# Optimization experiments

Hardware: AMD Instinct MI355X
Metric: run time of the kernel (lower is better)

Reference implementation:

```python
import jax, jax.numpy as jnp
import numpy as np
from jax import lax

B, T, N, HID = 4, 144, 256, 64
CH, NC = 9, 4  # chunk_size_short, num_chunks_short


def setup_inputs():
    key = jax.random.key(0)
    ks = jax.random.split(key, 30)
    r = lambda i, sh, s=0.05: jax.random.normal(ks[i], sh, jnp.float32) * s
    adj = (jax.random.uniform(ks[1], (N, N)) < 0.1).astype(jnp.float32)
    adj = adj.at[jnp.arange(N), jnp.arange(N)].set(1.0)  # self-loops
    return {
        "seg": jax.random.normal(ks[0], (B, T, N, N), jnp.float32),
        "adj": adj,
        "dist": jax.random.uniform(ks[2], (N, N), jnp.float32),
        "W_gat": r(3, (N, HID)),
        "a_src": r(4, (HID,)),
        "a_dst": r(5, (HID,)),
        "lstm_Wih": r(6, (4 * HID, HID)),
        "lstm_Whh": r(7, (4 * HID, HID)),
        "lstm_bih": r(8, (4 * HID,)),
        "lstm_bhh": r(9, (4 * HID,)),
        "attnL_W": r(10, (HID, HID)),
        "attnL_b": r(11, (HID,)),
        "attnL_v": r(12, (HID,)),
        "gru_Wih": r(13, (NC, 3 * HID, HID)),
        "gru_Whh": r(14, (NC, 3 * HID, HID)),
        "gru_bih": r(15, (NC, 3 * HID)),
        "gru_bhh": r(16, (NC, 3 * HID)),
        "attnS_W": r(17, (NC, HID, HID)),
        "attnS_b": r(18, (NC, HID)),
        "attnS_v": r(19, (NC, HID)),
        "lin1_W": r(20, (2 * HID, HID + HID * NC)),
        "lin1_b": r(21, (2 * HID,)),
        "lin2_W": r(22, (N * N, 2 * HID)),
        "lin2_b": r(23, (N * N,)),
        "conv_k": r(24, (1, 1, 3, 3)),
        "conv_b": r(25, (1,)),
    }


def gat_features(seg, adj, dist, W_gat, a_src, a_dst):
    # Batches the per-timestep GAT over the time axis (B,T folded together).
    Wh = jnp.einsum('btnf,fh->btnh', seg, W_gat)                     # (B,T,N,H)
    e = jax.nn.leaky_relu((Wh @ a_src)[..., :, None] + (Wh @ a_dst)[..., None, :], 0.2)
    e = e - dist                                                     # distance penalty on logits
    logits = jnp.where(adj > 0, e, -1e9)                             # mask non-edges
    attn = jax.nn.softmax(logits, axis=-1)                           # (B,T,N,N)
    Hn = jax.nn.elu(jnp.einsum('btij,btjh->btih', attn, Wh))         # (B,T,N,H)
    return Hn.mean(axis=2)                                           # (B,T,H) mean-pool over nodes


def lstm(x, Wih, Whh, bih, bhh):
    h0 = jnp.zeros((x.shape[0], Whh.shape[1]), x.dtype)
    def step(carry, xt):
        h, c = carry
        g = xt @ Wih.T + bih + h @ Whh.T + bhh
        i, f, gg, o = jnp.split(g, 4, axis=-1)  # torch gate order i,f,g,o
        c = jax.nn.sigmoid(f) * c + jax.nn.sigmoid(i) * jnp.tanh(gg)
        h = jax.nn.sigmoid(o) * jnp.tanh(c)
        return (h, c), h
    _, ys = lax.scan(step, (h0, h0), jnp.swapaxes(x, 0, 1))
    return jnp.swapaxes(ys, 0, 1)


def gru(x, Wih, Whh, bih, bhh):
    h0 = jnp.zeros((x.shape[0], Whh.shape[1]), x.dtype)
    def step(h, xt):
        gx = xt @ Wih.T + bih
        gh = h @ Whh.T + bhh
        xr, xz, xn = jnp.split(gx, 3, axis=-1)  # torch gate order r,z,n
        hr, hz, hn = jnp.split(gh, 3, axis=-1)
        rr = jax.nn.sigmoid(xr + hr)
        zz = jax.nn.sigmoid(xz + hz)
        nn_ = jnp.tanh(xn + rr * hn)
        h = (1.0 - zz) * nn_ + zz * h
        return h, h
    _, ys = lax.scan(step, h0, jnp.swapaxes(x, 0, 1))
    return jnp.swapaxes(ys, 0, 1)


def tattn(h, W, b, v):
    s = jnp.tanh(h @ W + b) @ v          # (B,T) additive attention scores
    a = jax.nn.softmax(s, axis=1)
    return jnp.einsum('bt,bth->bh', a, h)


def reference(seg, adj, dist, W_gat, a_src, a_dst, lstm_Wih, lstm_Whh, lstm_bih, lstm_bhh,
              attnL_W, attnL_b, attnL_v, gru_Wih, gru_Whh, gru_bih, gru_bhh,
              attnS_W, attnS_b, attnS_v, lin1_W, lin1_b, lin2_W, lin2_b, conv_k, conv_b):
    Bsz = seg.shape[0]
    feats = gat_features(seg, adj, dist, W_gat, a_src, a_dst)        # (B,T,H)
    ctxL = tattn(lstm(feats, lstm_Wih, lstm_Whh, lstm_bih, lstm_bhh), attnL_W, attnL_b, attnL_v)
    # Short-term GCN features are the same GAT outputs on the last W_short steps.
    short = feats[:, -CH * NC:, :].reshape(Bsz, NC, CH, HID)
    gru_out = jax.vmap(gru, in_axes=(1, 0, 0, 0, 0), out_axes=1)(short, gru_Wih, gru_Whh, gru_bih, gru_bhh)
    ctxS = jax.vmap(tattn, in_axes=(1, 0, 0, 0), out_axes=1)(gru_out, attnS_W, attnS_b, attnS_v)  # (B,NC,H)
    fused = jnp.concatenate([ctxL, ctxS.reshape(Bsz, NC * HID)], axis=1)  # (B, 5H)
    h1 = jax.nn.relu(fused @ lin1_W.T + lin1_b)
    out = (h1 @ lin2_W.T + lin2_b).reshape(Bsz, 1, N, N)
    out = lax.conv_general_dilated(out, conv_k, (1, 1), 'SAME',
                                   dimension_numbers=('NCHW', 'OIHW', 'NCHW'))
    out = out + conv_b[None, :, None, None]
    return jax.nn.softplus(out[:, 0])
```

## Files before the change

kernel.cpp:

```cpp
#include <hip/hip_runtime.h>
#include <hip/hip_bf16.h>
#include <cstddef>


typedef __attribute__((ext_vector_type(8))) short bf16x8;
typedef __attribute__((ext_vector_type(4))) float f32x4;

__device__ __forceinline__ float sigf(float x) { return 1.0f / (1.0f + __expf(-x)); }
__device__ __forceinline__ float tanh_(float x) {
    x = fminf(fmaxf(x, -15.f), 15.f);
    float e = __expf(2.f * x);
    return (e - 1.f) / (e + 1.f);
}
__device__ __forceinline__ unsigned short f2b(float f) {
    unsigned u = __float_as_uint(f);
    u += 0x7FFFu + ((u >> 16) & 1u);
    return (unsigned short)(u >> 16);
}
__device__ __forceinline__ unsigned pk2(float lo, float hi) {
    __hip_bfloat162 h = __float22bfloat162_rn(float2{lo, hi});
    return *reinterpret_cast<unsigned*>(&h);
}
__device__ __forceinline__ float b2f(short s) {
    return __uint_as_float(((unsigned)(unsigned short)s) << 16);
}
__device__ __forceinline__ float rlane(float v, int k) {
    return __uint_as_float(__builtin_amdgcn_readlane(__float_as_uint(v), k));
}

__global__ void k_prep(const float* __restrict__ adj, const float* __restrict__ dist,
                       const float* __restrict__ W_gat,
                       unsigned short* __restrict__ Mb, unsigned short* __restrict__ Wt) {
    int blk = blockIdx.x, tid = threadIdx.x;
    if (blk < 256) {
        int i = blk * 256 + tid;
        Mb[i] = f2b((adj[i] > 0.f) ? -dist[i] : -1e9f);
    } else {
        for (int it = 0; it < 64; ++it) {
            int e = it * 256 + tid;
            int k = e >> 6, c = e & 63;
            Wt[c * 256 + k] = f2b(W_gat[e]);
        }
    }
}

__global__ __launch_bounds__(256, 6) void k_gatA(
    const float* __restrict__ seg, const unsigned short* __restrict__ Wt,
    const float* __restrict__ a_src, const float* __restrict__ a_dst,
    unsigned short* __restrict__ WhT, float* __restrict__ svec, float* __restrict__ dvec,
    float* __restrict__ smaxp, float* __restrict__ dmaxp) {
    __shared__ __align__(16) short A_s[64 * 64];
    __shared__ float red[8];

    const int tid  = threadIdx.x;
    const int lane = tid & 63;
    const int wv   = tid >> 6;
    const int blk  = blockIdx.x;
    const int bt   = blk >> 2;
    const int sub  = blk & 3;
    const float* __restrict__ segp = seg + (size_t)bt * 65536 + sub * 64 * 256;

    f32x4 acc[4];
    #pragma unroll
    for (int n = 0; n < 4; ++n) acc[n] = (f32x4)(0.f);

    for (int kc = 0; kc < 4; ++kc) {
        #pragma unroll
        for (int it = 0; it < 2; ++it) {
            int unit = it * 256 + tid;
            int row = unit >> 3, u = unit & 7;
            const float* g = segp + row * 256 + kc * 64 + u * 8;
            f32x4 v0 = *(const f32x4*)g;
            f32x4 v1 = *(const f32x4*)(g + 4);
            uint4 pk;
            pk.x = pk2(v0[0], v0[1]); pk.y = pk2(v0[2], v0[3]);
            pk.z = pk2(v1[0], v1[1]); pk.w = pk2(v1[2], v1[3]);
            *(uint4*)&A_s[(row * 8 + (u ^ (row & 7))) * 8] = pk;
        }
        bf16x8 bfr[2][4];
        #pragma unroll
        for (int kt2 = 0; kt2 < 2; ++kt2) {
            int ku = kt2 * 4 + (lane >> 4);
            #pragma unroll
            for (int nt = 0; nt < 4; ++nt) {
                int col = nt * 16 + (lane & 15);
                bfr[kt2][nt] = *(const bf16x8*)(Wt + col * 256 + kc * 64 + ku * 8);
            }
        }
        __syncthreads();
        int arow = wv * 16 + (lane & 15);
        #pragma unroll
        for (int kt2 = 0; kt2 < 2; ++kt2) {
            int ku = kt2 * 4 + (lane >> 4);
            bf16x8 afr = *(const bf16x8*)&A_s[(arow * 8 + (ku ^ (arow & 7))) * 8];
            #pragma unroll
            for (int nt = 0; nt < 4; ++nt)
                acc[nt] = __builtin_amdgcn_mfma_f32_16x16x32_bf16(afr, bfr[kt2][nt], acc[nt], 0, 0, 0);
        }
        __syncthreads();
    }

    float asv[4], adv[4];
    #pragma unroll
    for (int nt = 0; nt < 4; ++nt) {
        asv[nt] = a_src[nt * 16 + (lane & 15)];
        adv[nt] = a_dst[nt * 16 + (lane & 15)];
    }
    float mxs = -3e38f, mxd = -3e38f;
    int rowbase = sub * 64 + wv * 16;
    #pragma unroll
    for (int r = 0; r < 4; ++r) {
        float ps = acc[0][r] * asv[0] + acc[1][r] * asv[1] + acc[2][r] * asv[2] + acc[3][r] * asv[3];
        float pd = acc[0][r] * adv[0] + acc[1][r] * adv[1] + acc[2][r] * adv[2] + acc[3][r] * adv[3];
        #pragma unroll
        for (int m = 1; m < 16; m <<= 1) { ps += __shfl_xor(ps, m); pd += __shfl_xor(pd, m); }
        if ((lane & 15) == 0) {
            int row = rowbase + (lane >> 4) * 4 + r;
            svec[bt * 256 + row] = ps;
            dvec[bt * 256 + row] = pd;
        }
        mxs = fmaxf(mxs, ps); mxd = fmaxf(mxd, pd);
    }
    mxs = fmaxf(mxs, __shfl_xor(mxs, 16)); mxs = fmaxf(mxs, __shfl_xor(mxs, 32));
    mxd = fmaxf(mxd, __shfl_xor(mxd, 16)); mxd = fmaxf(mxd, __shfl_xor(mxd, 32));
    if (lane == 0) { red[wv] = mxs; red[4 + wv] = mxd; }

    {
        int c = lane & 15, q = lane >> 4;
        int kt2  = wv >> 1;
        int oct  = (wv & 1) * 2 + (q >> 1);
        int laneP = oct * 16 + c;
        int e0b  = (q & 1) * 8;
        #pragma unroll
        for (int nt = 0; nt < 4; ++nt) {
            uint2 pk4;
            pk4.x = pk2(acc[nt][0], acc[nt][1]);
            pk4.y = pk2(acc[nt][2], acc[nt][3]);
            *(uint2*)((char*)A_s + (((kt2 * 4 + nt) * 64 + laneP) * 16 + e0b)) = pk4;
        }
    }
    __syncthreads();
    {
        const uint4* Fs = (const uint4*)A_s;
        uint4* Gd = (uint4*)(WhT + (size_t)bt * 16384 + sub * 4096);
        Gd[tid] = Fs[tid];
        Gd[256 + tid] = Fs[256 + tid];
    }
    if (tid == 0) {
        smaxp[blk] = fmaxf(fmaxf(red[0], red[1]), fmaxf(red[2], red[3]));
        dmaxp[blk] = fmaxf(fmaxf(red[4], red[5]), fmaxf(red[6], red[7]));
    }
}

__global__ __launch_bounds__(256, 4) void k_gatB(
    const unsigned short* __restrict__ WhT, const float* __restrict__ svec,
    const float* __restrict__ dvec, const float* __restrict__ smaxp,
    const float* __restrict__ dmaxp, const unsigned short* __restrict__ Mb,
    float* __restrict__ fpart) {
    __shared__ __align__(16) float dv_l[256];
    __shared__ float red[256];

    const int tid  = threadIdx.x;
    const int lane = tid & 63;
    const int wv   = tid >> 6;
    const int blk  = blockIdx.x;
    const int bt   = blk >> 2;
    const int sub  = blk & 3;
    const unsigned short* __restrict__ Wp = WhT + (size_t)bt * 16384;

    dv_l[tid] = dvec[bt * 256 + tid];
    float mB;
    {
        float ms = fmaxf(fmaxf(smaxp[bt * 4], smaxp[bt * 4 + 1]),
                         fmaxf(smaxp[bt * 4 + 2], smaxp[bt * 4 + 3]));
        float md = fmaxf(fmaxf(dmaxp[bt * 4], dmaxp[bt * 4 + 1]),
                         fmaxf(dmaxp[bt * 4 + 2], dmaxp[bt * 4 + 3]));
        float x = ms + md;
        mB = fmaxf(x, 0.2f * x);
    }
    const int prow = sub * 64 + wv * 16 + (lane & 15);
    const float sv = svec[bt * 256 + prow];
    __syncthreads();

    f32x4 acc2[4];
    #pragma unroll
    for (int n = 0; n < 4; ++n) acc2[n] = (f32x4)(0.f);
    float psum = 0.f;
    const int jbase = (lane >> 4) * 8;

    #pragma unroll 1
    for (int kt = 0; kt < 8; ++kt) {
        int j0 = kt * 32 + jbase;
        bf16x8 bfr[4];
        #pragma unroll
        for (int nt = 0; nt < 4; ++nt)
            bfr[nt] = *(const bf16x8*)(Wp + ((kt * 4 + nt) * 64 + lane) * 8);
        bf16x8 mrow = *(const bf16x8*)(Mb + prow * 256 + j0);
        f32x4 d0 = *(const f32x4*)&dv_l[j0];
        f32x4 d1 = *(const f32x4*)&dv_l[j0 + 4];
        float p[8];
        #pragma unroll
        for (int e = 0; e < 4; ++e) {
            float u = sv + d0[e];
            u = fmaxf(u, 0.2f * u);
            p[e] = __expf(u + b2f(mrow[e]) - mB);
            float w = sv + d1[e];
            w = fmaxf(w, 0.2f * w);
            p[4 + e] = __expf(w + b2f(mrow[4 + e]) - mB);
        }
        psum += ((p[0] + p[1]) + (p[2] + p[3])) + ((p[4] + p[5]) + (p[6] + p[7]));
        uint4 upf;
        upf.x = pk2(p[0], p[1]); upf.y = pk2(p[2], p[3]);
        upf.z = pk2(p[4], p[5]); upf.w = pk2(p[6], p[7]);
        bf16x8 pf = *reinterpret_cast<bf16x8*>(&upf);
        #pragma unroll
        for (int nt = 0; nt < 4; ++nt)
            acc2[nt] = __builtin_amdgcn_mfma_f32_16x16x32_bf16(pf, bfr[nt], acc2[nt], 0, 0, 0);
    }
    psum += __shfl_xor(psum, 16);
    psum += __shfl_xor(psum, 32);

    float part[4] = {0.f, 0.f, 0.f, 0.f};
    #pragma unroll
    for (int r = 0; r < 4; ++r) {
        float rs  = __shfl(psum, ((lane >> 4) << 2) + r);
        float inv = 1.0f / rs;
        #pragma unroll
        for (int nt = 0; nt < 4; ++nt) {
            float x = acc2[nt][r] * inv;
            x = (x > 0.f) ? x : expm1f(x);
            part[nt] += x;
        }
    }
    #pragma unroll
    for (int nt = 0; nt < 4; ++nt) {
        part[nt] += __shfl_xor(part[nt], 16);
        part[nt] += __shfl_xor(part[nt], 32);
    }
    if ((lane >> 4) == 0) {
        #pragma unroll
        for (int nt = 0; nt < 4; ++nt) red[wv * 64 + nt * 16 + lane] = part[nt];
    }
    __syncthreads();
    if (tid < 64)
        fpart[blk * 64 + tid] = red[tid] + red[64 + tid] + red[128 + tid] + red[192 + tid];
}

__global__ __launch_bounds__(256) void k_feats(
    const float* __restrict__ fpart, const float* __restrict__ lWih,
    const float* __restrict__ lbih, const float* __restrict__ lbhh,
    float* __restrict__ feats, float* __restrict__ gx) {
    __shared__ __align__(16) float fl[64];
    int bt = blockIdx.x, tid = threadIdx.x;
    if (tid < 64) {
        float f = (fpart[(bt * 4 + 0) * 64 + tid] + fpart[(bt * 4 + 1) * 64 + tid]
                 + fpart[(bt * 4 + 2) * 64 + tid] + fpart[(bt * 4 + 3) * 64 + tid]) * (1.0f / 256.0f);
        feats[bt * 64 + tid] = f;
        fl[tid] = f;
    }
    __syncthreads();
    float a = lbih[tid] + lbhh[tid];
    const float* wp = lWih + tid * 64;
    #pragma unroll
    for (int k4 = 0; k4 < 16; ++k4) {
        f32x4 w = *(const f32x4*)(wp + k4 * 4);
        f32x4 x = *(const f32x4*)&fl[k4 * 4];
        a += w[0] * x[0] + w[1] * x[1] + w[2] * x[2] + w[3] * x[3];
    }
    gx[bt * 256 + tid] = a;
}

__global__ __launch_bounds__(256) void k_rnn(
    const float* __restrict__ gx, const float* __restrict__ lWhh, float* __restrict__ lout,
    const float* __restrict__ feats, const float* __restrict__ gWih,
    const float* __restrict__ gWhh, const float* __restrict__ gbih,
    const float* __restrict__ gbhh, float* __restrict__ gout) {
    int tid = threadIdx.x;
    if (blockIdx.x < 4) {
        int b = blockIdx.x;
        int lane = tid & 63;
        __shared__ __align__(16) float gl[2][256];
        float wr[64];
        #pragma unroll
        for (int q = 0; q < 16; ++q)
            *(f32x4*)&wr[q * 4] = *(const f32x4*)&lWhh[tid * 64 + q * 4];
        float c_s = 0.f;
        float hprev = 0.f;
        float gx_cur = gx[(size_t)b * 36864 + tid];
        for (int t = 0; t < 144; ++t) {
            float gx_next = (t < 143) ? gx[((size_t)b * 144 + t + 1) * 256 + tid] : 0.f;
            float s0 = 0.f, s1 = 0.f, s2 = 0.f, s3 = 0.f;
            #pragma unroll
            for (int k = 0; k < 64; k += 4) {
                s0 += wr[k]     * rlane(hprev, k);
                s1 += wr[k + 1] * rlane(hprev, k + 1);
                s2 += wr[k + 2] * rlane(hprev, k + 2);
                s3 += wr[k + 3] * rlane(hprev, k + 3);
            }
            float a = gx_cur + ((s0 + s1) + (s2 + s3));
            gl[t & 1][tid] = a;
            __syncthreads();
            float ig = gl[t & 1][lane],       fg = gl[t & 1][64 + lane],
                  gg = gl[t & 1][128 + lane], og = gl[t & 1][192 + lane];
            c_s = sigf(fg) * c_s + sigf(ig) * tanh_(gg);
            float h = sigf(og) * tanh_(c_s);
            hprev = h;
            if (tid < 64) lout[(b * 144 + t) * 64 + lane] = h;
            gx_cur = gx_next;
        }
    } else {
        int bi_ = blockIdx.x - 4;
        int b = bi_ >> 2, c2 = bi_ & 3;
        __shared__ float hvg[64], xvg[64], gxl[192], ghl[192];
        float wi[64], wh[64], bi = 0.f, bh = 0.f, h_s = 0.f;
        if (tid < 192) {
            #pragma unroll
            for (int q = 0; q < 16; ++q) {
                *(f32x4*)&wi[q * 4] = *(const f32x4*)&gWih[(size_t)(c2 * 192 + tid) * 64 + q * 4];
                *(f32x4*)&wh[q * 4] = *(const f32x4*)&gWhh[(size_t)(c2 * 192 + tid) * 64 + q * 4];
            }
            bi = gbih[c2 * 192 + tid];
            bh = gbhh[c2 * 192 + tid];
        }
        if (tid < 64) hvg[tid] = 0.f;
        __syncthreads();
        for (int s = 0; s < 9; ++s) {
            int t = 108 + c2 * 9 + s;
            if (tid < 64) xvg[tid] = feats[(b * 144 + t) * 64 + tid];
            __syncthreads();
            if (tid < 192) {
                float ax = bi, ah = bh;
                float a0 = 0.f, a1 = 0.f, b0 = 0.f, b1 = 0.f;
                #pragma unroll
                for (int k = 0; k < 64; k += 2) {
                    a0 += wi[k] * xvg[k];     a1 += wi[k + 1] * xvg[k + 1];
                    b0 += wh[k] * hvg[k];     b1 += wh[k + 1] * hvg[k + 1];
                }
                gxl[tid] = ax + a0 + a1; ghl[tid] = ah + b0 + b1;
            }
            __syncthreads();
            if (tid < 64) {
                float xr = gxl[tid], xz = gxl[64 + tid], xn = gxl[128 + tid];
                float hr = ghl[tid], hz = ghl[64 + tid], hn = ghl[128 + tid];
                float rr = sigf(xr + hr), zz = sigf(xz + hz);
                float nn = tanh_(xn + rr * hn);
                h_s = (1.f - zz) * nn + zz * h_s;
                hvg[tid] = h_s;
                gout[((b * 4 + c2) * 9 + s) * 64 + tid] = h_s;
            }
            __syncthreads();
        }
    }
}

__global__ __launch_bounds__(256) void k_ctx(
    const float* __restrict__ lout, const float* __restrict__ aLW,
    const float* __restrict__ aLb, const float* __restrict__ aLv,
    const float* __restrict__ gout, const float* __restrict__ aSW,
    const float* __restrict__ aSb, const float* __restrict__ aSv,
    float* __restrict__ ctxL, float* __restrict__ ctxS) {
    int tid = threadIdx.x;
    if (blockIdx.x < 4) {
        int b = blockIdx.x;
        int wv = tid >> 6, lane = tid & 63;
        __shared__ __align__(16) float Hl[144 * 64];
        __shared__ float sc[144];
        __shared__ float al[144];
        for (int i = tid; i < 9216; i += 256) Hl[i] = lout[b * 9216 + i];
        float wcol[64];
        #pragma unroll
        for (int k = 0; k < 64; ++k) wcol[k] = aLW[k * 64 + lane];
        float bb = aLb[lane], vv = aLv[lane];
        __syncthreads();
        for (int g = 0; g < 36; ++g) {
            int t = g * 4 + wv;
            float acc = bb;
            #pragma unroll
            for (int q = 0; q < 16; ++q) {
                f32x4 h4 = *(const f32x4*)&Hl[t * 64 + q * 4];
                acc += wcol[q * 4 + 0] * h4[0] + wcol[q * 4 + 1] * h4[1]
                     + wcol[q * 4 + 2] * h4[2] + wcol[q * 4 + 3] * h4[3];
            }
            float p = tanh_(acc) * vv;
            #pragma unroll
            for (int m = 1; m < 64; m <<= 1) p += __shfl_xor(p, m);
            if (lane == 0) sc[t] = p;
        }
        __syncthreads();
        float mx = -3e38f;
        for (int t2 = 0; t2 < 144; ++t2) mx = fmaxf(mx, sc[t2]);
        float ss = 0.f;
        for (int t2 = 0; t2 < 144; ++t2) ss += __expf(sc[t2] - mx);
        float inv = 1.f / ss;
        if (tid < 144) al[tid] = __expf(sc[tid] - mx) * inv;
        __syncthreads();
        if (tid < 64) {
            float acc = 0.f;
            for (int t2 = 0; t2 < 144; ++t2) acc += al[t2] * Hl[t2 * 64 + tid];
            ctxL[b * 64 + tid] = acc;
        }
    } else {
        int bi_ = blockIdx.x - 4;
        int b = bi_ >> 2, c2 = bi_ & 3;
        __shared__ float xv2[64];
        if (tid < 64) {
            int lane = tid;
            const float* Wc = aSW + c2 * 4096;
            float wcol[64];
            #pragma unroll
            for (int k = 0; k < 64; ++k) wcol[k] = Wc[k * 64 + lane];
            float bb = aSb[c2 * 64 + lane], vv = aSv[c2 * 64 + lane];
            float sv[9], hl[9];
            #pragma unroll 1
            for (int s = 0; s < 9; ++s) {
                float h = gout[((size_t)((b * 4 + c2) * 9 + s)) * 64 + lane];
                hl[s] = h;
                xv2[lane] = h;
                float acc = bb;
                #pragma unroll
                for (int k = 0; k < 64; ++k) acc += wcol[k] * xv2[k];
                float p = tanh_(acc) * vv;
                #pragma unroll
                for (int m = 1; m < 64; m <<= 1) p += __shfl_xor(p, m);
                sv[s] = p;
            }
            float mx = -3e38f;
            #pragma unroll
            for (int s = 0; s < 9; ++s) mx = fmaxf(mx, sv[s]);
            float ss = 0.f;
            #pragma unroll
            for (int s = 0; s < 9; ++s) { sv[s] = __expf(sv[s] - mx); ss += sv[s]; }
            float inv = 1.f / ss;
            float acc = 0.f;
            #pragma unroll
            for (int s = 0; s < 9; ++s) acc += sv[s] * inv * hl[s];
            ctxS[(b * 4 + c2) * 64 + lane] = acc;
        }
    }
}

__global__ __launch_bounds__(512) void k_lin1(
    const float* __restrict__ ctxL, const float* __restrict__ ctxS,
    const float* __restrict__ W, const float* __restrict__ bb,
    float* __restrict__ h1) {
    int tid = threadIdx.x;
    __shared__ __align__(16) float fu[4 * 320];
    for (int c = tid; c < 1280; c += 512) {
        int b2 = c / 320, k = c % 320;
        fu[c] = (k < 64) ? ctxL[b2 * 64 + k] : ctxS[b2 * 256 + (k - 64)];
    }
    __syncthreads();
    int b = tid >> 7, r = tid & 127;
    float acc = bb[r];
    #pragma unroll 4
    for (int k4 = 0; k4 < 80; ++k4) {
        f32x4 w = *(const f32x4*)&W[r * 320 + k4 * 4];
        f32x4 x = *(const f32x4*)&fu[b * 320 + k4 * 4];
        acc += w[0] * x[0] + w[1] * x[1] + w[2] * x[2] + w[3] * x[3];
    }
    h1[b * 128 + r] = fmaxf(acc, 0.f);
}

__global__ __launch_bounds__(256) void k_lin2(
    const float* __restrict__ h1, const float* __restrict__ W,
    const float* __restrict__ bb, float* __restrict__ h2) {
    __shared__ __align__(16) float h1l[512];
    int tid = threadIdx.x, blk = blockIdx.x;
    for (int c = tid; c < 512; c += 256) h1l[c] = h1[c];
    __syncthreads();
    int r = blk * 64 + (tid >> 2);
    int q = tid & 3;
    const float* wp = W + (size_t)r * 128 + q * 32;
    float a0 = 0.f, a1 = 0.f, a2 = 0.f, a3 = 0.f;
    #pragma unroll
    for (int i = 0; i < 8; ++i) {
        f32x4 w  = *(const f32x4*)(wp + i * 4);
        f32x4 x0 = *(const f32x4*)&h1l[q * 32 + i * 4];
        f32x4 x1 = *(const f32x4*)&h1l[128 + q * 32 + i * 4];
        f32x4 x2 = *(const f32x4*)&h1l[256 + q * 32 + i * 4];
        f32x4 x3 = *(const f32x4*)&h1l[384 + q * 32 + i * 4];
        a0 += w[0] * x0[0] + w[1] * x0[1] + w[2] * x0[2] + w[3] * x0[3];
        a1 += w[0] * x1[0] + w[1] * x1[1] + w[2] * x1[2] + w[3] * x1[3];
        a2 += w[0] * x2[0] + w[1] * x2[1] + w[2] * x2[2] + w[3] * x2[3];
        a3 += w[0] * x3[0] + w[1] * x3[1] + w[2] * x3[2] + w[3] * x3[3];
    }
    a0 += __shfl_xor(a0, 1); a0 += __shfl_xor(a0, 2);
    a1 += __shfl_xor(a1, 1); a1 += __shfl_xor(a1, 2);
    a2 += __shfl_xor(a2, 1); a2 += __shfl_xor(a2, 2);
    a3 += __shfl_xor(a3, 1); a3 += __shfl_xor(a3, 2);
    if (q == 0) {
        float bv = bb[r];
        h2[r]             = a0 + bv;
        h2[65536 + r]     = a1 + bv;
        h2[2 * 65536 + r] = a2 + bv;
        h2[3 * 65536 + r] = a3 + bv;
    }
}

__global__ __launch_bounds__(256) void k_conv(
    const float* __restrict__ h2, const float* __restrict__ ck,
    const float* __restrict__ cb, float* __restrict__ out) {
    int x = threadIdx.x;
    int b = blockIdx.x >> 8, y = blockIdx.x & 255;
    float kk[9];
    #pragma unroll
    for (int i = 0; i < 9; ++i) kk[i] = ck[i];
    const float* base = h2 + b * 65536;
    float acc = cb[0];
    #pragma unroll
    for (int dy = -1; dy <= 1; ++dy) {
        int yy = y + dy;
        if (yy < 0 || yy > 255) continue;
        #pragma unroll
        for (int dx = -1; dx <= 1; ++dx) {
            int xx = x + dx;
            if (xx < 0 || xx > 255) continue;
            acc += base[yy * 256 + xx] * kk[(dy + 1) * 3 + (dx + 1)];
        }
    }
    float r = (acc > 20.f) ? acc : log1pf(__expf(acc));
    out[b * 65536 + y * 256 + x] = r;
}

extern "C" void kernel_launch(void* const* d_in, const int* in_sizes, int n_in,
                              void* d_out, int out_size, void* d_ws, size_t ws_size,
                              hipStream_t stream) {
    const float* seg   = (const float*)d_in[0];
    const float* adj   = (const float*)d_in[1];
    const float* dist  = (const float*)d_in[2];
    const float* W_gat = (const float*)d_in[3];
    const float* a_src = (const float*)d_in[4];
    const float* a_dst = (const float*)d_in[5];
    const float* lWih  = (const float*)d_in[6];
    const float* lWhh  = (const float*)d_in[7];
    const float* lbih  = (const float*)d_in[8];
    const float* lbhh  = (const float*)d_in[9];
    const float* aLW   = (const float*)d_in[10];
    const float* aLb   = (const float*)d_in[11];
    const float* aLv   = (const float*)d_in[12];
    const float* gWih  = (const float*)d_in[13];
    const float* gWhh  = (const float*)d_in[14];
    const float* gbih  = (const float*)d_in[15];
    const float* gbhh  = (const float*)d_in[16];
    const float* aSW   = (const float*)d_in[17];
    const float* aSb   = (const float*)d_in[18];
    const float* aSv   = (const float*)d_in[19];
    const float* l1W   = (const float*)d_in[20];
    const float* l1b   = (const float*)d_in[21];
    const float* l2W   = (const float*)d_in[22];
    const float* l2b   = (const float*)d_in[23];
    const float* ck    = (const float*)d_in[24];
    const float* cb    = (const float*)d_in[25];
    float* out = (float*)d_out;

    float* ws = (float*)d_ws;
    unsigned short* Mb  = (unsigned short*)ws;
    unsigned short* Wt  = (unsigned short*)(ws + 32768);
    float* svec  = ws + 40960;
    float* dvec  = svec + 147456;
    float* smaxp = dvec + 147456;
    float* dmaxp = smaxp + 2304;
    unsigned short* WhT = (unsigned short*)(dmaxp + 2304);
    float* fpart = dmaxp + 2304 + 4718592;
    float* feats = fpart + 147456;
    float* gx    = feats + 36864;
    float* lout  = gx + 147456;
    float* gout  = lout + 36864;
    float* ctxL  = gout + 9216;
    float* ctxS  = ctxL + 256;
    float* h1    = ctxS + 1024;
    float* h2    = h1 + 512;

    k_prep<<<257, 256, 0, stream>>>(adj, dist, W_gat, Mb, Wt);
    k_gatA<<<2304, 256, 0, stream>>>(seg, Wt, a_src, a_dst, WhT, svec, dvec, smaxp, dmaxp);
    k_gatB<<<2304, 256, 0, stream>>>(WhT, svec, dvec, smaxp, dmaxp, Mb, fpart);
    k_feats<<<576, 256, 0, stream>>>(fpart, lWih, lbih, lbhh, feats, gx);
    k_rnn<<<20, 256, 0, stream>>>(gx, lWhh, lout, feats, gWih, gWhh, gbih, gbhh, gout);
    k_ctx<<<20, 256, 0, stream>>>(lout, aLW, aLb, aLv, gout, aSW, aSb, aSv, ctxL, ctxS);
    k_lin1<<<1, 512, 0, stream>>>(ctxL, ctxS, l1W, l1b, h1);
    k_lin2<<<1024, 256, 0, stream>>>(h1, l2W, l2b, h2);
    k_conv<<<1024, 256, 0, stream>>>(h2, ck, cb, out);
}
```

Measured before the change: 231.4 us.

## Fuse GAT aggregation with LSTM input projection, and RNN with attention context

```diff
diff --git a/kernel.cpp b/kernel.cpp
--- a/kernel.cpp
+++ b/kernel.cpp
@@ -152,20 +152,21 @@
     }
 }
 
-__global__ __launch_bounds__(256, 4) void k_gatB(
+__global__ __launch_bounds__(256, 4) void k_gatBF(
     const unsigned short* __restrict__ WhT, const float* __restrict__ svec,
     const float* __restrict__ dvec, const float* __restrict__ smaxp,
     const float* __restrict__ dmaxp, const unsigned short* __restrict__ Mb,
-    float* __restrict__ fpart) {
+    const float* __restrict__ lWih, const float* __restrict__ lbih,
+    const float* __restrict__ lbhh, float* __restrict__ feats, float* __restrict__ gx) {
     __shared__ __align__(16) float dv_l[256];
     __shared__ float red[256];
+    __shared__ __align__(16) float feats_l[64];
 
     const int tid  = threadIdx.x;
     const int lane = tid & 63;
     const int wv   = tid >> 6;
-    const int blk  = blockIdx.x;
-    const int bt   = blk >> 2;
-    const int sub  = blk & 3;
+    const int wrow = wv * 64;
+    const int bt   = blockIdx.x;
     const unsigned short* __restrict__ Wp = WhT + (size_t)bt * 16384;
 
     dv_l[tid] = dvec[bt * 256 + tid];
@@ -178,14 +179,17 @@
         float x = ms + md;
         mB = fmaxf(x, 0.2f * x);
     }
-    const int prow = sub * 64 + wv * 16 + (lane & 15);
-    const float sv = svec[bt * 256 + prow];
+    float sv4[4];
+    #pragma unroll
+    for (int mt = 0; mt < 4; ++mt) sv4[mt] = svec[bt * 256 + wrow + mt * 16 + (lane & 15)];
     __syncthreads();
 
-    f32x4 acc2[4];
-    #pragma unroll
-    for (int n = 0; n < 4; ++n) acc2[n] = (f32x4)(0.f);
-    float psum = 0.f;
+    f32x4 acc2[4][4];
+    #pragma unroll
+    for (int a = 0; a < 4; ++a)
+        #pragma unroll
+        for (int b = 0; b < 4; ++b) acc2[a][b] = (f32x4)(0.f);
+    float psum[4] = {0.f, 0.f, 0.f, 0.f};
     const int jbase = (lane >> 4) * 8;
 
     #pragma unroll 1
@@ -195,41 +199,51 @@
         #pragma unroll
         for (int nt = 0; nt < 4; ++nt)
             bfr[nt] = *(const bf16x8*)(Wp + ((kt * 4 + nt) * 64 + lane) * 8);
-        bf16x8 mrow = *(const bf16x8*)(Mb + prow * 256 + j0);
         f32x4 d0 = *(const f32x4*)&dv_l[j0];
         f32x4 d1 = *(const f32x4*)&dv_l[j0 + 4];
-        float p[8];
-        #pragma unroll
-        for (int e = 0; e < 4; ++e) {
-            float u = sv + d0[e];
-            u = fmaxf(u, 0.2f * u);
-            p[e] = __expf(u + b2f(mrow[e]) - mB);
-            float w = sv + d1[e];
-            w = fmaxf(w, 0.2f * w);
-            p[4 + e] = __expf(w + b2f(mrow[4 + e]) - mB);
-        }
-        psum += ((p[0] + p[1]) + (p[2] + p[3])) + ((p[4] + p[5]) + (p[6] + p[7]));
-        uint4 upf;
-        upf.x = pk2(p[0], p[1]); upf.y = pk2(p[2], p[3]);
-        upf.z = pk2(p[4], p[5]); upf.w = pk2(p[6], p[7]);
-        bf16x8 pf = *reinterpret_cast<bf16x8*>(&upf);
-        #pragma unroll
-        for (int nt = 0; nt < 4; ++nt)
-            acc2[nt] = __builtin_amdgcn_mfma_f32_16x16x32_bf16(pf, bfr[nt], acc2[nt], 0, 0, 0);
-    }
-    psum += __shfl_xor(psum, 16);
-    psum += __shfl_xor(psum, 32);
+        #pragma unroll
+        for (int mt = 0; mt < 4; ++mt) {
+            int prow = wrow + mt * 16 + (lane & 15);
+            bf16x8 mrow = *(const bf16x8*)(Mb + prow * 256 + j0);
+            float p[8];
+            #pragma unroll
+            for (int e = 0; e < 4; ++e) {
+                float u = sv4[mt] + d0[e];
+                u = fmaxf(u, 0.2f * u);
+                p[e] = __expf(u + b2f(mrow[e]) - mB);
+                float w = sv4[mt] + d1[e];
+                w = fmaxf(w, 0.2f * w);
+                p[4 + e] = __expf(w + b2f(mrow[4 + e]) - mB);
+            }
+            psum[mt] += ((p[0] + p[1]) + (p[2] + p[3])) + ((p[4] + p[5]) + (p[6] + p[7]));
+            uint4 upf;
+            upf.x = pk2(p[0], p[1]); upf.y = pk2(p[2], p[3]);
+            upf.z = pk2(p[4], p[5]); upf.w = pk2(p[6], p[7]);
+            bf16x8 pf = *reinterpret_cast<bf16x8*>(&upf);
+            #pragma unroll
+            for (int nt = 0; nt < 4; ++nt)
+                acc2[mt][nt] = __builtin_amdgcn_mfma_f32_16x16x32_bf16(pf, bfr[nt], acc2[mt][nt], 0, 0, 0);
+        }
+    }
+    #pragma unroll
+    for (int mt = 0; mt < 4; ++mt) {
+        psum[mt] += __shfl_xor(psum[mt], 16);
+        psum[mt] += __shfl_xor(psum[mt], 32);
+    }
 
     float part[4] = {0.f, 0.f, 0.f, 0.f};
     #pragma unroll
-    for (int r = 0; r < 4; ++r) {
-        float rs  = __shfl(psum, ((lane >> 4) << 2) + r);
-        float inv = 1.0f / rs;
-        #pragma unroll
-        for (int nt = 0; nt < 4; ++nt) {
-            float x = acc2[nt][r] * inv;
-            x = (x > 0.f) ? x : expm1f(x);
-            part[nt] += x;
+    for (int mt = 0; mt < 4; ++mt) {
+        #pragma unroll
+        for (int r = 0; r < 4; ++r) {
+            float rs  = __shfl(psum[mt], ((lane >> 4) << 2) + r);
+            float inv = 1.0f / rs;
+            #pragma unroll
+            for (int nt = 0; nt < 4; ++nt) {
+                float x = acc2[mt][nt][r] * inv;
+                x = (x > 0.f) ? x : expm1f(x);
+                part[nt] += x;
+            }
         }
     }
     #pragma unroll
@@ -242,44 +256,42 @@
         for (int nt = 0; nt < 4; ++nt) red[wv * 64 + nt * 16 + lane] = part[nt];
     }
     __syncthreads();
-    if (tid < 64)
-        fpart[blk * 64 + tid] = red[tid] + red[64 + tid] + red[128 + tid] + red[192 + tid];
-}
-
-__global__ __launch_bounds__(256) void k_feats(
-    const float* __restrict__ fpart, const float* __restrict__ lWih,
-    const float* __restrict__ lbih, const float* __restrict__ lbhh,
-    float* __restrict__ feats, float* __restrict__ gx) {
-    __shared__ __align__(16) float fl[64];
-    int bt = blockIdx.x, tid = threadIdx.x;
     if (tid < 64) {
-        float f = (fpart[(bt * 4 + 0) * 64 + tid] + fpart[(bt * 4 + 1) * 64 + tid]
-                 + fpart[(bt * 4 + 2) * 64 + tid] + fpart[(bt * 4 + 3) * 64 + tid]) * (1.0f / 256.0f);
+        float f = (red[tid] + red[64 + tid] + red[128 + tid] + red[192 + tid]) * (1.0f / 256.0f);
         feats[bt * 64 + tid] = f;
-        fl[tid] = f;
+        feats_l[tid] = f;
     }
     __syncthreads();
-    float a = lbih[tid] + lbhh[tid];
-    const float* wp = lWih + tid * 64;
-    #pragma unroll
-    for (int k4 = 0; k4 < 16; ++k4) {
-        f32x4 w = *(const f32x4*)(wp + k4 * 4);
-        f32x4 x = *(const f32x4*)&fl[k4 * 4];
-        a += w[0] * x[0] + w[1] * x[1] + w[2] * x[2] + w[3] * x[3];
-    }
-    gx[bt * 256 + tid] = a;
-}
-
-__global__ __launch_bounds__(256) void k_rnn(
-    const float* __restrict__ gx, const float* __restrict__ lWhh, float* __restrict__ lout,
+    {
+        float a = lbih[tid] + lbhh[tid];
+        const float* wp = lWih + tid * 64;
+        #pragma unroll
+        for (int k4 = 0; k4 < 16; ++k4) {
+            f32x4 w = *(const f32x4*)(wp + k4 * 4);
+            f32x4 x = *(const f32x4*)&feats_l[k4 * 4];
+            a += w[0] * x[0] + w[1] * x[1] + w[2] * x[2] + w[3] * x[3];
+        }
+        gx[bt * 256 + tid] = a;
+    }
+}
+
+__global__ __launch_bounds__(256) void k_rnnctx(
+    const float* __restrict__ gx, const float* __restrict__ lWhh,
+    const float* __restrict__ aLW, const float* __restrict__ aLb, const float* __restrict__ aLv,
     const float* __restrict__ feats, const float* __restrict__ gWih,
     const float* __restrict__ gWhh, const float* __restrict__ gbih,
-    const float* __restrict__ gbhh, float* __restrict__ gout) {
+    const float* __restrict__ gbhh, const float* __restrict__ aSW,
+    const float* __restrict__ aSb, const float* __restrict__ aSv,
+    float* __restrict__ ctxL, float* __restrict__ ctxS) {
+    __shared__ __align__(16) float smem[10048];
     int tid = threadIdx.x;
     if (blockIdx.x < 4) {
         int b = blockIdx.x;
-        int lane = tid & 63;
-        __shared__ __align__(16) float gl[2][256];
+        int lane = tid & 63, wv = tid >> 6;
+        float* Hl = smem;
+        float* gl = smem + 9216;
+        float* sc = smem + 9728;
+        float* al = smem + 9872;
         float wr[64];
         #pragma unroll
         for (int q = 0; q < 16; ++q)
@@ -298,20 +310,56 @@
                 s3 += wr[k + 3] * rlane(hprev, k + 3);
             }
             float a = gx_cur + ((s0 + s1) + (s2 + s3));
-            gl[t & 1][tid] = a;
+            gl[(t & 1) * 256 + tid] = a;
             __syncthreads();
-            float ig = gl[t & 1][lane],       fg = gl[t & 1][64 + lane],
-                  gg = gl[t & 1][128 + lane], og = gl[t & 1][192 + lane];
+            float ig = gl[(t & 1) * 256 + lane],       fg = gl[(t & 1) * 256 + 64 + lane],
+                  gg = gl[(t & 1) * 256 + 128 + lane], og = gl[(t & 1) * 256 + 192 + lane];
             c_s = sigf(fg) * c_s + sigf(ig) * tanh_(gg);
             float h = sigf(og) * tanh_(c_s);
             hprev = h;
-            if (tid < 64) lout[(b * 144 + t) * 64 + lane] = h;
+            if (wv == 0) Hl[t * 64 + lane] = h;
             gx_cur = gx_next;
+        }
+        __syncthreads();
+        float wcol[64];
+        #pragma unroll
+        for (int k = 0; k < 64; ++k) wcol[k] = aLW[k * 64 + lane];
+        float bb = aLb[lane], vv = aLv[lane];
+        for (int g = 0; g < 36; ++g) {
+            int t = g * 4 + wv;
+            float acc = bb;
+            #pragma unroll
+            for (int q = 0; q < 16; ++q) {
+                f32x4 h4 = *(const f32x4*)&Hl[t * 64 + q * 4];
+                acc += wcol[q * 4 + 0] * h4[0] + wcol[q * 4 + 1] * h4[1]
+                     + wcol[q * 4 + 2] * h4[2] + wcol[q * 4 + 3] * h4[3];
+            }
+            float p = tanh_(acc) * vv;
+            #pragma unroll
+            for (int m = 1; m < 64; m <<= 1) p += __shfl_xor(p, m);
+            if (lane == 0) sc[t] = p;
+        }
+        __syncthreads();
+        float mx = -3e38f;
+        for (int t2 = 0; t2 < 144; ++t2) mx = fmaxf(mx, sc[t2]);
+        float ss = 0.f;
+        for (int t2 = 0; t2 < 144; ++t2) ss += __expf(sc[t2] - mx);
+        float inv = 1.f / ss;
+        if (tid < 144) al[tid] = __expf(sc[tid] - mx) * inv;
+        __syncthreads();
+        if (tid < 64) {
+            float acc = 0.f;
+            for (int t2 = 0; t2 < 144; ++t2) acc += al[t2] * Hl[t2 * 64 + tid];
+            ctxL[b * 64 + tid] = acc;
         }
     } else {
         int bi_ = blockIdx.x - 4;
         int b = bi_ >> 2, c2 = bi_ & 3;
-        __shared__ float hvg[64], xvg[64], gxl[192], ghl[192];
+        float* hvg = smem;
+        float* xvg = smem + 64;
+        float* gxl = smem + 128;
+        float* ghl = smem + 320;
+        float* hst = smem + 512;
         float wi[64], wh[64], bi = 0.f, bh = 0.f, h_s = 0.f;
         if (tid < 192) {
             #pragma unroll
@@ -346,63 +394,10 @@
                 float nn = tanh_(xn + rr * hn);
                 h_s = (1.f - zz) * nn + zz * h_s;
                 hvg[tid] = h_s;
-                gout[((b * 4 + c2) * 9 + s) * 64 + tid] = h_s;
+                hst[s * 64 + tid] = h_s;
             }
             __syncthreads();
         }
-    }
-}
-
-__global__ __launch_bounds__(256) void k_ctx(
-    const float* __restrict__ lout, const float* __restrict__ aLW,
-    const float* __restrict__ aLb, const float* __restrict__ aLv,
-    const float* __restrict__ gout, const float* __restrict__ aSW,
-    const float* __restrict__ aSb, const float* __restrict__ aSv,
-    float* __restrict__ ctxL, float* __restrict__ ctxS) {
-    int tid = threadIdx.x;
-    if (blockIdx.x < 4) {
-        int b = blockIdx.x;
-        int wv = tid >> 6, lane = tid & 63;
-        __shared__ __align__(16) float Hl[144 * 64];
-        __shared__ float sc[144];
-        __shared__ float al[144];
-        for (int i = tid; i < 9216; i += 256) Hl[i] = lout[b * 9216 + i];
-        float wcol[64];
-        #pragma unroll
-        for (int k = 0; k < 64; ++k) wcol[k] = aLW[k * 64 + lane];
-        float bb = aLb[lane], vv = aLv[lane];
-        __syncthreads();
-        for (int g = 0; g < 36; ++g) {
-            int t = g * 4 + wv;
-            float acc = bb;
-            #pragma unroll
-            for (int q = 0; q < 16; ++q) {
-                f32x4 h4 = *(const f32x4*)&Hl[t * 64 + q * 4];
-                acc += wcol[q * 4 + 0] * h4[0] + wcol[q * 4 + 1] * h4[1]
-                     + wcol[q * 4 + 2] * h4[2] + wcol[q * 4 + 3] * h4[3];
-            }
-            float p = tanh_(acc) * vv;
-            #pragma unroll
-            for (int m = 1; m < 64; m <<= 1) p += __shfl_xor(p, m);
-            if (lane == 0) sc[t] = p;
-        }
-        __syncthreads();
-        float mx = -3e38f;
-        for (int t2 = 0; t2 < 144; ++t2) mx = fmaxf(mx, sc[t2]);
-        float ss = 0.f;
-        for (int t2 = 0; t2 < 144; ++t2) ss += __expf(sc[t2] - mx);
-        float inv = 1.f / ss;
-        if (tid < 144) al[tid] = __expf(sc[tid] - mx) * inv;
-        __syncthreads();
-        if (tid < 64) {
-            float acc = 0.f;
-            for (int t2 = 0; t2 < 144; ++t2) acc += al[t2] * Hl[t2 * 64 + tid];
-            ctxL[b * 64 + tid] = acc;
-        }
-    } else {
-        int bi_ = blockIdx.x - 4;
-        int b = bi_ >> 2, c2 = bi_ & 3;
-        __shared__ float xv2[64];
         if (tid < 64) {
             int lane = tid;
             const float* Wc = aSW + c2 * 4096;
@@ -410,15 +405,16 @@
             #pragma unroll
             for (int k = 0; k < 64; ++k) wcol[k] = Wc[k * 64 + lane];
             float bb = aSb[c2 * 64 + lane], vv = aSv[c2 * 64 + lane];
-            float sv[9], hl[9];
+            float sv[9];
             #pragma unroll 1
             for (int s = 0; s < 9; ++s) {
-                float h = gout[((size_t)((b * 4 + c2) * 9 + s)) * 64 + lane];
-                hl[s] = h;
-                xv2[lane] = h;
                 float acc = bb;
                 #pragma unroll
-                for (int k = 0; k < 64; ++k) acc += wcol[k] * xv2[k];
+                for (int q = 0; q < 16; ++q) {
+                    f32x4 h4 = *(const f32x4*)&hst[s * 64 + q * 4];
+                    acc += wcol[q * 4 + 0] * h4[0] + wcol[q * 4 + 1] * h4[1]
+                         + wcol[q * 4 + 2] * h4[2] + wcol[q * 4 + 3] * h4[3];
+                }
                 float p = tanh_(acc) * vv;
                 #pragma unroll
                 for (int m = 1; m < 64; m <<= 1) p += __shfl_xor(p, m);
@@ -433,7 +429,7 @@
             float inv = 1.f / ss;
             float acc = 0.f;
             #pragma unroll
-            for (int s = 0; s < 9; ++s) acc += sv[s] * inv * hl[s];
+            for (int s = 0; s < 9; ++s) acc += sv[s] * inv * hst[s * 64 + lane];
             ctxS[(b * 4 + c2) * 64 + lane] = acc;
         }
     }
@@ -561,22 +557,18 @@
     float* smaxp = dvec + 147456;
     float* dmaxp = smaxp + 2304;
     unsigned short* WhT = (unsigned short*)(dmaxp + 2304);
-    float* fpart = dmaxp + 2304 + 4718592;
-    float* feats = fpart + 147456;
+    float* feats = dmaxp + 2304 + 4718592;
     float* gx    = feats + 36864;
-    float* lout  = gx + 147456;
-    float* gout  = lout + 36864;
-    float* ctxL  = gout + 9216;
+    float* ctxL  = gx + 147456;
     float* ctxS  = ctxL + 256;
     float* h1    = ctxS + 1024;
     float* h2    = h1 + 512;
 
     k_prep<<<257, 256, 0, stream>>>(adj, dist, W_gat, Mb, Wt);
     k_gatA<<<2304, 256, 0, stream>>>(seg, Wt, a_src, a_dst, WhT, svec, dvec, smaxp, dmaxp);
-    k_gatB<<<2304, 256, 0, stream>>>(WhT, svec, dvec, smaxp, dmaxp, Mb, fpart);
-    k_feats<<<576, 256, 0, stream>>>(fpart, lWih, lbih, lbhh, feats, gx);
-    k_rnn<<<20, 256, 0, stream>>>(gx, lWhh, lout, feats, gWih, gWhh, gbih, gbhh, gout);
-    k_ctx<<<20, 256, 0, stream>>>(lout, aLW, aLb, aLv, gout, aSW, aSb, aSv, ctxL, ctxS);
+    k_gatBF<<<576, 256, 0, stream>>>(WhT, svec, dvec, smaxp, dmaxp, Mb, lWih, lbih, lbhh, feats, gx);
+    k_rnnctx<<<20, 256, 0, stream>>>(gx, lWhh, aLW, aLb, aLv, feats, gWih, gWhh, gbih, gbhh,
+                                     aSW, aSb, aSv, ctxL, ctxS);
     k_lin1<<<1, 512, 0, stream>>>(ctxL, ctxS, l1W, l1b, h1);
     k_lin2<<<1024, 256, 0, stream>>>(h1, l2W, l2b, h2);
     k_conv<<<1024, 256, 0, stream>>>(h2, ck, cb, out);
```

After: 236.7 us. 2.3% more time.
